# Performance work log

Hardware: AMD Instinct MI355X
Metric: run time of the kernel (lower is better)

## Reference

```python
import jax, jax.numpy as jnp
import numpy as np


def setup_inputs() -> dict:
    key = jax.random.key(0)
    ks = jax.random.split(key, 8)
    B, N, D, S = 4, 16384, 512, 512
    x = jax.random.normal(ks[0], (B, N, D), dtype=jnp.float32)
    jx = jnp.sort(jax.random.randint(ks[1], (N,), 0, S, dtype=jnp.int64))
    scale = 1.0 / np.sqrt(D)
    Wf = jax.random.normal(ks[2], (D, D), dtype=jnp.float32) * scale
    bf = jax.random.normal(ks[3], (D,), dtype=jnp.float32) * scale
    Wg = jax.random.normal(ks[4], (D, D), dtype=jnp.float32) * scale
    bg = jax.random.normal(ks[5], (D,), dtype=jnp.float32) * scale
    Wh = jax.random.normal(ks[6], (D, D), dtype=jnp.float32) * scale
    bh = jax.random.normal(ks[7], (D,), dtype=jnp.float32) * scale
    return {"x": x, "jx": jx, "num_segments": S, "Wf": Wf, "bf": bf,
            "Wg": Wg, "bg": bg, "Wh": Wh, "bh": bh}


def reference(x, jx, num_segments, Wf, bf, Wg, bg, Wh, bh):
    # x: [B, N, D]; jx: [N] segment ids; segments along axis 1.
    fx = jnp.einsum('bnd,ed->bne', x, Wf) + bf  # f(x)
    gx = jnp.einsum('bnd,ed->bne', x, Wg) + bg  # g(x)
    # move N to leading axis so jax.ops.segment_* apply: [N, B, D]
    gx_t = jnp.transpose(gx, (1, 0, 2))
    fx_t = jnp.transpose(fx, (1, 0, 2))
    # scatter_softmax over segments (numerically stable)
    m = jax.ops.segment_max(gx_t, jx, num_segments=num_segments)  # [S, B, D]
    e = jnp.exp(gx_t - m[jx])
    denom = jax.ops.segment_sum(e, jx, num_segments=num_segments)  # [S, B, D]
    w = e / denom[jx]  # [N, B, D]
    # weighted scatter-sum
    y_t = jax.ops.segment_sum(fx_t * w, jx, num_segments=num_segments)  # [S, B, D]
    y = jnp.transpose(y_t, (1, 0, 2))  # [B, S, D]
    hy = jnp.einsum('bsd,ed->bse', y, Wh) + bh
    # expand=True: gather back to per-element
    return hy[:, jx]  # [B, N, D]
```

## Files before the change

kernel.cpp:

```cpp
#include <hip/hip_runtime.h>
#include <stdint.h>

#define B_ 4
#define N_ 16384
#define D_ 512
#define S_ 512

typedef __attribute__((ext_vector_type(8))) short bf16x8;
typedef __attribute__((ext_vector_type(4))) float f32x4;

__device__ __forceinline__ float bf2f(unsigned short u) {
  union { unsigned int i; float f; } v; v.i = ((unsigned int)u) << 16; return v.f;
}
__device__ __forceinline__ unsigned short f2bf(float f) {
  unsigned int x = __float_as_uint(f);
  return (unsigned short)((x + 0x7FFFu + ((x >> 16) & 1u)) >> 16);
}
__device__ __forceinline__ float ldf(const void* p, long i, bool f32) {
  return f32 ? ((const float*)p)[i] : bf2f(((const unsigned short*)p)[i]);
}
__device__ __forceinline__ void gl_lds16(void* lds_base, const void* g) {
  __builtin_amdgcn_global_load_lds(
      (const __attribute__((address_space(1))) unsigned int*)g,
      (__attribute__((address_space(3))) unsigned int*)lds_base,
      16, 0, 0);
}

__device__ __forceinline__ bool jx_is_i64(const int* jx32) { return jx32[N_ - 1] == 0; }
__device__ __forceinline__ int seg_id(const int* jx32, int n, bool i64) {
  return i64 ? jx32[2 * n] : jx32[n];
}

__global__ void detect_f32(const unsigned short* __restrict__ x, int* __restrict__ flag) {
  __shared__ int cnt[256];
  int c = 0;
#pragma unroll
  for (int i = 0; i < 8; i++) {
    unsigned short w = x[threadIdx.x * 8 + i];
    int e = (w >> 7) & 0xFF;
    if (e == 0 || (e >= 100 && e <= 140)) c++;
  }
  cnt[threadIdx.x] = c;
  __syncthreads();
  for (int s = 128; s > 0; s >>= 1) {
    if ((int)threadIdx.x < s) cnt[threadIdx.x] += cnt[threadIdx.x + s];
    __syncthreads();
  }
  if (threadIdx.x == 0) *flag = (cnt[0] < (2048 * 9) / 10) ? 1 : 0;
}

__global__ void seg_bounds(const int* __restrict__ jx, int* __restrict__ st) {
  int s = blockIdx.x * blockDim.x + threadIdx.x;
  if (s > S_) return;
  bool i64 = jx_is_i64(jx);
  int lo = 0, hi = N_;
  while (lo < hi) {
    int mid = (lo + hi) >> 1;
    if (seg_id(jx, mid, i64) < s) lo = mid + 1; else hi = mid;
  }
  st[s] = lo;
}

__global__ void prep(const void* __restrict__ Wf, const void* __restrict__ bfv,
                     const void* __restrict__ Wg, const void* __restrict__ bgv,
                     const void* __restrict__ Wh, const void* __restrict__ bhv,
                     const int* __restrict__ flag,
                     unsigned short* __restrict__ Wfg, unsigned short* __restrict__ biasfg,
                     unsigned short* __restrict__ Whb, unsigned short* __restrict__ bhb) {
  const bool f32 = *flag != 0;
  int idx = blockIdx.x * 256 + threadIdx.x;
  if (idx < 524288) {
    int e = idx >> 9, d = idx & 511;
    float v = (e < 512) ? ldf(Wf, (long)e * 512 + d, f32)
                        : ldf(Wg, (long)(e - 512) * 512 + d, f32);
    Wfg[idx] = f2bf(v);
  } else if (idx < 786432) {
    Whb[idx - 524288] = f2bf(ldf(Wh, idx - 524288, f32));
  } else if (idx < 787456) {
    int j = idx - 786432;
    biasfg[j] = f2bf(j < 512 ? ldf(bfv, j, f32) : ldf(bgv, j - 512, f32));
  } else if (idx < 787968) {
    bhb[idx - 787456] = f2bf(ldf(bhv, idx - 787456, f32));
  }
}

__global__ __launch_bounds__(256)
void cvt_x(const void* __restrict__ x, const int* __restrict__ flag,
           unsigned short* __restrict__ xb) {
  const bool f32 = *flag != 0;
  const size_t i0 = ((size_t)blockIdx.x * 256 + threadIdx.x) * 8;
  bf16x8 v;
  if (f32) {
    const float4* p = (const float4*)((const float*)x + i0);
    float4 a = p[0], b = p[1];
    v[0]=f2bf(a.x); v[1]=f2bf(a.y); v[2]=f2bf(a.z); v[3]=f2bf(a.w);
    v[4]=f2bf(b.x); v[5]=f2bf(b.y); v[6]=f2bf(b.z); v[7]=f2bf(b.w);
  } else {
    v = *(const bf16x8*)((const unsigned short*)x + i0);
  }
  *(bf16x8*)(xb + i0) = v;
}

#define BK 32

__global__ __launch_bounds__(256, 2)
void gemm_bt(const unsigned short* __restrict__ A, const unsigned short* __restrict__ Bm,
             const unsigned short* __restrict__ bias,
             unsigned short* __restrict__ Cf, unsigned short* __restrict__ Cg,
             int E, int Kdim, int splitcol, int tilesM, int tilesN) {
  __shared__ __align__(16) unsigned short As[128 * BK];
  __shared__ __align__(16) unsigned short Bs[128 * BK];
  const int L = blockIdx.x;
  const int xcd = L & 7, local = L >> 3;
  const int rowsPerX = tilesM >> 3;
  const int tm = xcd * rowsPerX + local / tilesN;
  const int tn = local % tilesN;
  const int m0 = tm * 128, n0 = tn * 128;

  const int tid  = threadIdx.x;
  const int w    = tid >> 6;
  const int lane = tid & 63;
  const int wm   = w >> 1, wn = w & 1;
  const int l15  = lane & 15, l4 = lane >> 4;
  const int srow = lane >> 2;
  const int scol = (lane & 3) * 8;

  f32x4 acc[4][4];
#pragma unroll
  for (int i = 0; i < 4; i++)
#pragma unroll
    for (int j = 0; j < 4; j++) acc[i][j] = (f32x4){0.f, 0.f, 0.f, 0.f};

  for (int kt = 0; kt < Kdim; kt += BK) {
    __syncthreads();
#pragma unroll
    for (int r = 0; r < 2; r++) {
      const int rb = (r * 4 + w) * 16;
      gl_lds16(&As[rb * BK], A + (size_t)(m0 + rb + srow) * Kdim + kt + scol);
      gl_lds16(&Bs[rb * BK], Bm + (size_t)(n0 + rb + srow) * Kdim + kt + scol);
    }
    __syncthreads();

    bf16x8 a[4], b[4];
#pragma unroll
    for (int i = 0; i < 4; i++)
      a[i] = *(const bf16x8*)&As[(wm * 64 + i * 16 + l15) * BK + l4 * 8];
#pragma unroll
    for (int j = 0; j < 4; j++)
      b[j] = *(const bf16x8*)&Bs[(wn * 64 + j * 16 + l15) * BK + l4 * 8];
#pragma unroll
    for (int i = 0; i < 4; i++)
#pragma unroll
      for (int j = 0; j < 4; j++)
        acc[i][j] = __builtin_amdgcn_mfma_f32_16x16x32_bf16(a[i], b[j], acc[i][j], 0, 0, 0);
  }

#pragma unroll
  for (int j = 0; j < 4; j++) {
    const int col = n0 + wn * 64 + j * 16 + l15;
    const float bv = bf2f(bias[col]);
    unsigned short* base; int cc, stride;
    if (col < splitcol) { base = Cf; cc = col; stride = splitcol; }
    else { base = Cg; cc = col - splitcol; stride = E - splitcol; }
#pragma unroll
    for (int i = 0; i < 4; i++) {
      const int rowb = m0 + wm * 64 + i * 16 + l4 * 4;
#pragma unroll
      for (int r = 0; r < 4; r++)
        base[(size_t)(rowb + r) * stride + cc] = f2bf(acc[i][j][r] + bv);
    }
  }
}

__global__ __launch_bounds__(256)
void seg_softmax(const unsigned short* __restrict__ f, const unsigned short* __restrict__ g,
                 const int* __restrict__ segst, unsigned short* __restrict__ y) {
  const int s = blockIdx.x, b = blockIdx.y;
  const int st = segst[s], en = segst[s + 1];
  const int d0 = threadIdx.x * 2;
  float den0 = 0.f, den1 = 0.f, y0 = 0.f, y1 = 0.f;
  for (int n = st; n < en; n++) {
    const size_t off = (size_t)(b * N_ + n) * 512 + d0;
    const unsigned int fp = *(const unsigned int*)(f + off);
    const unsigned int gp = *(const unsigned int*)(g + off);
    const float f0 = bf2f((unsigned short)fp), f1 = bf2f((unsigned short)(fp >> 16));
    const float g0 = bf2f((unsigned short)gp), g1 = bf2f((unsigned short)(gp >> 16));
    const float e0 = __expf(g0), e1 = __expf(g1);
    den0 += e0; den1 += e1;
    y0 += f0 * e0; y1 += f1 * e1;
  }
  const float r0 = (en > st) ? y0 / den0 : 0.f;
  const float r1 = (en > st) ? y1 / den1 : 0.f;
  unsigned short* yr = y + (size_t)(b * S_ + s) * 512 + d0;
  yr[0] = f2bf(r0);
  yr[1] = f2bf(r1);
}

__global__ __launch_bounds__(256)
void gather_out(const unsigned short* __restrict__ hy, const int* __restrict__ jx,
                void* __restrict__ out, const int* __restrict__ flag) {
  const bool f32 = *flag != 0;
  const int gid  = blockIdx.x * 256 + threadIdx.x;
  const int wid  = gid >> 6;
  const int lane = gid & 63;
  const int b = wid >> 14;
  const int n = wid & (N_ - 1);
  const bool i64 = jx_is_i64(jx);
  const int s = seg_id(jx, n, i64);
  const bf16x8 v = *(const bf16x8*)(hy + (size_t)(b * S_ + s) * 512 + lane * 8);
  if (f32) {
    float* dst = (float*)out + (size_t)wid * 512 + lane * 8;
#pragma unroll
    for (int t = 0; t < 8; t++) dst[t] = bf2f((unsigned short)v[t]);
  } else {
    *(bf16x8*)((unsigned short*)out + (size_t)wid * 512 + lane * 8) = v;
  }
}

extern "C" void kernel_launch(void* const* d_in, const int* in_sizes, int n_in,
                              void* d_out, int out_size, void* d_ws, size_t ws_size,
                              hipStream_t stream) {
  const void* x  = d_in[0];
  const int* jx  = (const int*)d_in[1];
  const void* Wf = d_in[3];
  const void* bf = d_in[4];
  const void* Wg = d_in[5];
  const void* bg = d_in[6];
  const void* Wh = d_in[7];
  const void* bh = d_in[8];

  char* ws = (char*)d_ws;
  int* flag              = (int*)(ws + 0);
  int* segst             = (int*)(ws + 4096);
  unsigned short* biasfg = (unsigned short*)(ws + 8192);
  unsigned short* bhb    = (unsigned short*)(ws + 16384);
  unsigned short* Wfg    = (unsigned short*)(ws + 32768);
  unsigned short* Whb    = (unsigned short*)(ws + 1081344);
  unsigned short* y_ws   = (unsigned short*)(ws + 1605632);
  unsigned short* hy_ws  = (unsigned short*)(ws + 3702784);
  unsigned short* xb     = (unsigned short*)(ws + 8388608);
  unsigned short* fbuf   = (unsigned short*)d_out;
  unsigned short* gbuf   = (unsigned short*)d_out + (size_t)B_ * N_ * D_;

  detect_f32<<<1, 256, 0, stream>>>((const unsigned short*)x, flag);
  seg_bounds<<<3, 256, 0, stream>>>(jx, segst);
  prep<<<3078, 256, 0, stream>>>(Wf, bf, Wg, bg, Wh, bh, flag, Wfg, biasfg, Whb, bhb);
  cvt_x<<<16384, 256, 0, stream>>>(x, flag, xb);
  gemm_bt<<<4096, 256, 0, stream>>>(xb, Wfg, biasfg, fbuf, gbuf,
                                    1024, 512, 512, 512, 8);
  seg_softmax<<<dim3(S_, B_), 256, 0, stream>>>(fbuf, gbuf, segst, y_ws);
  gemm_bt<<<64, 256, 0, stream>>>(y_ws, Whb, bhb, hy_ws, hy_ws,
                                  512, 512, 512, 16, 4);
  gather_out<<<16384, 256, 0, stream>>>(hy_ws, jx, d_out, flag);
}
```

Before: 399.1 us.

## Fuse segment softmax-weighted reduction into f/g GEMM epilogue with atomics

Interleaves the Wf and Wg rows so each GEMM tile holds matching f and g columns. The epilogue computes exp(g)*f and exp(g), reduces them per segment inside the tile and atomically adds them into a float numerator/denominator buffer. A small kernel then divides to form y. The aim is to stop writing and re-reading the full bf16 f and g intermediates and to drop the separate softmax pass. Detection, segment-bound and prep launches are also merged into one kernel. In exchange it adds a memset, atomic contention and a per-block dtype classification, and it drops the max subtraction, which was already absent before.

Measured after the change: 428.9 us. 7.5% more time.

```diff
diff --git a/kernel.cpp b/kernel.cpp
--- a/kernel.cpp
+++ b/kernel.cpp
@@ -26,13 +26,7 @@
       16, 0, 0);
 }
 
-__device__ __forceinline__ bool jx_is_i64(const int* jx32) { return jx32[N_ - 1] == 0; }
-__device__ __forceinline__ int seg_id(const int* jx32, int n, bool i64) {
-  return i64 ? jx32[2 * n] : jx32[n];
-}
-
-__global__ void detect_f32(const unsigned short* __restrict__ x, int* __restrict__ flag) {
-  __shared__ int cnt[256];
+__device__ __forceinline__ bool classify_f32(const unsigned short* x, int* cnt) {
   int c = 0;
 #pragma unroll
   for (int i = 0; i < 8; i++) {
@@ -46,76 +40,78 @@
     if ((int)threadIdx.x < s) cnt[threadIdx.x] += cnt[threadIdx.x + s];
     __syncthreads();
   }
-  if (threadIdx.x == 0) *flag = (cnt[0] < (2048 * 9) / 10) ? 1 : 0;
-}
-
-__global__ void seg_bounds(const int* __restrict__ jx, int* __restrict__ st) {
-  int s = blockIdx.x * blockDim.x + threadIdx.x;
-  if (s > S_) return;
-  bool i64 = jx_is_i64(jx);
-  int lo = 0, hi = N_;
-  while (lo < hi) {
-    int mid = (lo + hi) >> 1;
-    if (seg_id(jx, mid, i64) < s) lo = mid + 1; else hi = mid;
-  }
-  st[s] = lo;
-}
-
-__global__ void prep(const void* __restrict__ Wf, const void* __restrict__ bfv,
-                     const void* __restrict__ Wg, const void* __restrict__ bgv,
-                     const void* __restrict__ Wh, const void* __restrict__ bhv,
-                     const int* __restrict__ flag,
-                     unsigned short* __restrict__ Wfg, unsigned short* __restrict__ biasfg,
-                     unsigned short* __restrict__ Whb, unsigned short* __restrict__ bhb) {
-  const bool f32 = *flag != 0;
-  int idx = blockIdx.x * 256 + threadIdx.x;
-  if (idx < 524288) {
-    int e = idx >> 9, d = idx & 511;
-    float v = (e < 512) ? ldf(Wf, (long)e * 512 + d, f32)
-                        : ldf(Wg, (long)(e - 512) * 512 + d, f32);
-    Wfg[idx] = f2bf(v);
-  } else if (idx < 786432) {
-    Whb[idx - 524288] = f2bf(ldf(Wh, idx - 524288, f32));
-  } else if (idx < 787456) {
-    int j = idx - 786432;
-    biasfg[j] = f2bf(j < 512 ? ldf(bfv, j, f32) : ldf(bgv, j - 512, f32));
-  } else if (idx < 787968) {
-    bhb[idx - 787456] = f2bf(ldf(bhv, idx - 787456, f32));
-  }
+  bool f32 = cnt[0] < 1843;
+  __syncthreads();
+  return f32;
+}
+
+__device__ __forceinline__ bool jx_is_i64(const int* jx32) { return jx32[N_ - 1] == 0; }
+__device__ __forceinline__ int seg_id(const int* jx32, int n, bool i64) {
+  return i64 ? jx32[2 * n] : jx32[n];
 }
 
 __global__ __launch_bounds__(256)
-void cvt_x(const void* __restrict__ x, const int* __restrict__ flag,
-           unsigned short* __restrict__ xb) {
-  const bool f32 = *flag != 0;
-  const size_t i0 = ((size_t)blockIdx.x * 256 + threadIdx.x) * 8;
-  bf16x8 v;
-  if (f32) {
-    const float4* p = (const float4*)((const float*)x + i0);
-    float4 a = p[0], b = p[1];
-    v[0]=f2bf(a.x); v[1]=f2bf(a.y); v[2]=f2bf(a.z); v[3]=f2bf(a.w);
-    v[4]=f2bf(b.x); v[5]=f2bf(b.y); v[6]=f2bf(b.z); v[7]=f2bf(b.w);
+void prep_all(const void* __restrict__ x, const int* __restrict__ jx,
+              const void* __restrict__ Wf, const void* __restrict__ bfv,
+              const void* __restrict__ Wg, const void* __restrict__ bgv,
+              const void* __restrict__ Wh, const void* __restrict__ bhv,
+              unsigned short* __restrict__ xb, unsigned short* __restrict__ Wfg,
+              unsigned short* __restrict__ biasfg, unsigned short* __restrict__ Whb,
+              unsigned short* __restrict__ bhb) {
+  const int blk = blockIdx.x, tid = threadIdx.x;
+  __shared__ int cnt[256];
+  const bool f32 = classify_f32((const unsigned short*)x, cnt);
+  if (blk < 16384) {
+    const size_t i0 = ((size_t)blk * 256 + tid) * 8;
+    bf16x8 v;
+    if (f32) {
+      const float4* p = (const float4*)((const float*)x + i0);
+      float4 a = p[0], b = p[1];
+      v[0]=f2bf(a.x); v[1]=f2bf(a.y); v[2]=f2bf(a.z); v[3]=f2bf(a.w);
+      v[4]=f2bf(b.x); v[5]=f2bf(b.y); v[6]=f2bf(b.z); v[7]=f2bf(b.w);
+    } else {
+      v = *(const bf16x8*)((const unsigned short*)x + i0);
+    }
+    *(bf16x8*)(xb + i0) = v;
   } else {
-    v = *(const bf16x8*)((const unsigned short*)x + i0);
-  }
-  *(bf16x8*)(xb + i0) = v;
+    int idx = (blk - 16384) * 256 + tid;
+    if (idx < 524288) {
+      int e = idx >> 9, dcol = idx & 511;
+      int drow = e >> 1;
+      float v = (e & 1) ? ldf(Wg, (long)drow * 512 + dcol, f32)
+                        : ldf(Wf, (long)drow * 512 + dcol, f32);
+      Wfg[idx] = f2bf(v);
+    } else if (idx < 786432) {
+      Whb[idx - 524288] = f2bf(ldf(Wh, idx - 524288, f32));
+    } else if (idx < 787456) {
+      int j = idx - 786432;
+      biasfg[j] = f2bf((j & 1) ? ldf(bgv, j >> 1, f32) : ldf(bfv, j >> 1, f32));
+    } else if (idx < 787968) {
+      bhb[idx - 787456] = f2bf(ldf(bhv, idx - 787456, f32));
+    }
+  }
 }
 
 #define BK 32
 
 __global__ __launch_bounds__(256, 2)
-void gemm_bt(const unsigned short* __restrict__ A, const unsigned short* __restrict__ Bm,
-             const unsigned short* __restrict__ bias,
-             unsigned short* __restrict__ Cf, unsigned short* __restrict__ Cg,
-             int E, int Kdim, int splitcol, int tilesM, int tilesN) {
-  __shared__ __align__(16) unsigned short As[128 * BK];
-  __shared__ __align__(16) unsigned short Bs[128 * BK];
+void gemm_fg_fused(const unsigned short* __restrict__ A,
+                   const unsigned short* __restrict__ Bm,
+                   const unsigned short* __restrict__ bias,
+                   const int* __restrict__ jx,
+                   float* __restrict__ nd) {
+  __shared__ __align__(16) char smem[16384];
+  unsigned short* As = (unsigned short*)smem;
+  unsigned short* Bs = (unsigned short*)(smem + 8192);
+  float2* red = (float2*)smem;
+
   const int L = blockIdx.x;
   const int xcd = L & 7, local = L >> 3;
-  const int rowsPerX = tilesM >> 3;
-  const int tm = xcd * rowsPerX + local / tilesN;
-  const int tn = local % tilesN;
+  const int tm = xcd * 64 + local / 8;
+  const int tn = local % 8;
   const int m0 = tm * 128, n0 = tn * 128;
+  const int b = m0 >> 14;
+  const int nbase = m0 & (N_ - 1);
 
   const int tid  = threadIdx.x;
   const int w    = tid >> 6;
@@ -131,6 +127,106 @@
 #pragma unroll
     for (int j = 0; j < 4; j++) acc[i][j] = (f32x4){0.f, 0.f, 0.f, 0.f};
 
+  for (int kt = 0; kt < 512; kt += BK) {
+    __syncthreads();
+#pragma unroll
+    for (int r = 0; r < 2; r++) {
+      const int rb = (r * 4 + w) * 16;
+      gl_lds16(&As[rb * BK], A + (size_t)(m0 + rb + srow) * 512 + kt + scol);
+      gl_lds16(&Bs[rb * BK], Bm + (size_t)(n0 + rb + srow) * 512 + kt + scol);
+    }
+    __syncthreads();
+
+    bf16x8 a[4], bb[4];
+#pragma unroll
+    for (int i = 0; i < 4; i++)
+      a[i] = *(const bf16x8*)&As[(wm * 64 + i * 16 + l15) * BK + l4 * 8];
+#pragma unroll
+    for (int j = 0; j < 4; j++)
+      bb[j] = *(const bf16x8*)&Bs[(wn * 64 + j * 16 + l15) * BK + l4 * 8];
+#pragma unroll
+    for (int i = 0; i < 4; i++)
+#pragma unroll
+      for (int j = 0; j < 4; j++)
+        acc[i][j] = __builtin_amdgcn_mfma_f32_16x16x32_bf16(a[i], bb[j], acc[i][j], 0, 0, 0);
+  }
+
+  const bool i64 = jx_is_i64(jx);
+  const bool evenlane = (l15 & 1) == 0;
+  const int slot_w = wn * 8 + (l15 >> 1);
+  for (int j = 0; j < 4; j++) {
+    __syncthreads();
+    const int col = n0 + wn * 64 + j * 16 + l15;
+    const float bv = bf2f(bias[col]);
+#pragma unroll
+    for (int i = 0; i < 4; i++) {
+#pragma unroll
+      for (int r = 0; r < 4; r++) {
+        const float val = acc[i][j][r] + bv;
+        const float partner = __shfl_xor(val, 1);
+        if (evenlane) {
+          const float e = __expf(partner);
+          const int row = wm * 64 + i * 16 + l4 * 4 + r;
+          red[row * 16 + slot_w] = make_float2(val * e, e);
+        }
+      }
+    }
+    __syncthreads();
+    if (tid < 128) {
+      const int slot = tid & 15, chunk = tid >> 4;
+      const int dg = (n0 >> 1) + (slot >> 3) * 32 + j * 8 + (slot & 7);
+      const int rbase = chunk * 16;
+      float nsum = 0.f, dsum = 0.f;
+      int cur = seg_id(jx, nbase + rbase, i64);
+      for (int k = 0; k < 16; k++) {
+        const int sg = seg_id(jx, nbase + rbase + k, i64);
+        const float2 v = red[(rbase + k) * 16 + slot];
+        if (sg != cur) {
+          float* t = nd + (((size_t)(b * S_ + cur)) * 512 + dg) * 2;
+          atomicAdd(t, nsum); atomicAdd(t + 1, dsum);
+          nsum = 0.f; dsum = 0.f; cur = sg;
+        }
+        nsum += v.x; dsum += v.y;
+      }
+      float* t = nd + (((size_t)(b * S_ + cur)) * 512 + dg) * 2;
+      atomicAdd(t, nsum); atomicAdd(t + 1, dsum);
+    }
+  }
+}
+
+__global__ __launch_bounds__(256)
+void y_div(const float* __restrict__ nd, unsigned short* __restrict__ y) {
+  const size_t i0 = ((size_t)blockIdx.x * 256 + threadIdx.x) * 2;
+  const float4 v = *(const float4*)(nd + i0 * 2);
+  unsigned int o = (unsigned int)f2bf(v.y > 0.f ? v.x / v.y : 0.f)
+                 | ((unsigned int)f2bf(v.w > 0.f ? v.z / v.w : 0.f) << 16);
+  *(unsigned int*)(y + i0) = o;
+}
+
+__global__ __launch_bounds__(256, 2)
+void gemm_bt(const unsigned short* __restrict__ A, const unsigned short* __restrict__ Bm,
+             const unsigned short* __restrict__ bias, unsigned short* __restrict__ C,
+             int E, int Kdim, int tilesM, int tilesN) {
+  __shared__ __align__(16) unsigned short As[128 * BK];
+  __shared__ __align__(16) unsigned short Bs[128 * BK];
+  const int L = blockIdx.x;
+  const int xcd = L & 7, local = L >> 3;
+  const int tm = xcd * (tilesM >> 3) + local / tilesN;
+  const int tn = local % tilesN;
+  const int m0 = tm * 128, n0 = tn * 128;
+  const int tid  = threadIdx.x;
+  const int w    = tid >> 6;
+  const int lane = tid & 63;
+  const int wm   = w >> 1, wn = w & 1;
+  const int l15  = lane & 15, l4 = lane >> 4;
+  const int srow = lane >> 2, scol = (lane & 3) * 8;
+
+  f32x4 acc[4][4];
+#pragma unroll
+  for (int i = 0; i < 4; i++)
+#pragma unroll
+    for (int j = 0; j < 4; j++) acc[i][j] = (f32x4){0.f, 0.f, 0.f, 0.f};
+
   for (int kt = 0; kt < Kdim; kt += BK) {
     __syncthreads();
 #pragma unroll
@@ -140,66 +236,38 @@
       gl_lds16(&Bs[rb * BK], Bm + (size_t)(n0 + rb + srow) * Kdim + kt + scol);
     }
     __syncthreads();
-
-    bf16x8 a[4], b[4];
+    bf16x8 a[4], bb[4];
 #pragma unroll
     for (int i = 0; i < 4; i++)
       a[i] = *(const bf16x8*)&As[(wm * 64 + i * 16 + l15) * BK + l4 * 8];
 #pragma unroll
     for (int j = 0; j < 4; j++)
-      b[j] = *(const bf16x8*)&Bs[(wn * 64 + j * 16 + l15) * BK + l4 * 8];
+      bb[j] = *(const bf16x8*)&Bs[(wn * 64 + j * 16 + l15) * BK + l4 * 8];
 #pragma unroll
     for (int i = 0; i < 4; i++)
 #pragma unroll
       for (int j = 0; j < 4; j++)
-        acc[i][j] = __builtin_amdgcn_mfma_f32_16x16x32_bf16(a[i], b[j], acc[i][j], 0, 0, 0);
-  }
-
+        acc[i][j] = __builtin_amdgcn_mfma_f32_16x16x32_bf16(a[i], bb[j], acc[i][j], 0, 0, 0);
+  }
 #pragma unroll
   for (int j = 0; j < 4; j++) {
     const int col = n0 + wn * 64 + j * 16 + l15;
     const float bv = bf2f(bias[col]);
-    unsigned short* base; int cc, stride;
-    if (col < splitcol) { base = Cf; cc = col; stride = splitcol; }
-    else { base = Cg; cc = col - splitcol; stride = E - splitcol; }
 #pragma unroll
     for (int i = 0; i < 4; i++) {
       const int rowb = m0 + wm * 64 + i * 16 + l4 * 4;
 #pragma unroll
       for (int r = 0; r < 4; r++)
-        base[(size_t)(rowb + r) * stride + cc] = f2bf(acc[i][j][r] + bv);
-    }
-  }
-}
-
-__global__ __launch_bounds__(256)
-void seg_softmax(const unsigned short* __restrict__ f, const unsigned short* __restrict__ g,
-                 const int* __restrict__ segst, unsigned short* __restrict__ y) {
-  const int s = blockIdx.x, b = blockIdx.y;
-  const int st = segst[s], en = segst[s + 1];
-  const int d0 = threadIdx.x * 2;
-  float den0 = 0.f, den1 = 0.f, y0 = 0.f, y1 = 0.f;
-  for (int n = st; n < en; n++) {
-    const size_t off = (size_t)(b * N_ + n) * 512 + d0;
-    const unsigned int fp = *(const unsigned int*)(f + off);
-    const unsigned int gp = *(const unsigned int*)(g + off);
-    const float f0 = bf2f((unsigned short)fp), f1 = bf2f((unsigned short)(fp >> 16));
-    const float g0 = bf2f((unsigned short)gp), g1 = bf2f((unsigned short)(gp >> 16));
-    const float e0 = __expf(g0), e1 = __expf(g1);
-    den0 += e0; den1 += e1;
-    y0 += f0 * e0; y1 += f1 * e1;
-  }
-  const float r0 = (en > st) ? y0 / den0 : 0.f;
-  const float r1 = (en > st) ? y1 / den1 : 0.f;
-  unsigned short* yr = y + (size_t)(b * S_ + s) * 512 + d0;
-  yr[0] = f2bf(r0);
-  yr[1] = f2bf(r1);
+        C[(size_t)(rowb + r) * E + col] = f2bf(acc[i][j][r] + bv);
+    }
+  }
 }
 
 __global__ __launch_bounds__(256)
 void gather_out(const unsigned short* __restrict__ hy, const int* __restrict__ jx,
-                void* __restrict__ out, const int* __restrict__ flag) {
-  const bool f32 = *flag != 0;
+                void* __restrict__ out, const void* __restrict__ x) {
+  __shared__ int cnt[256];
+  const bool f32 = classify_f32((const unsigned short*)x, cnt);
   const int gid  = blockIdx.x * 256 + threadIdx.x;
   const int wid  = gid >> 6;
   const int lane = gid & 63;
@@ -210,8 +278,13 @@
   const bf16x8 v = *(const bf16x8*)(hy + (size_t)(b * S_ + s) * 512 + lane * 8);
   if (f32) {
     float* dst = (float*)out + (size_t)wid * 512 + lane * 8;
-#pragma unroll
-    for (int t = 0; t < 8; t++) dst[t] = bf2f((unsigned short)v[t]);
+    float4 lo, hi;
+    lo.x=bf2f((unsigned short)v[0]); lo.y=bf2f((unsigned short)v[1]);
+    lo.z=bf2f((unsigned short)v[2]); lo.w=bf2f((unsigned short)v[3]);
+    hi.x=bf2f((unsigned short)v[4]); hi.y=bf2f((unsigned short)v[5]);
+    hi.z=bf2f((unsigned short)v[6]); hi.w=bf2f((unsigned short)v[7]);
+    *(float4*)dst = lo;
+    *(float4*)(dst + 4) = hi;
   } else {
     *(bf16x8*)((unsigned short*)out + (size_t)wid * 512 + lane * 8) = v;
   }
@@ -230,26 +303,20 @@
   const void* bh = d_in[8];
 
   char* ws = (char*)d_ws;
-  int* flag              = (int*)(ws + 0);
-  int* segst             = (int*)(ws + 4096);
   unsigned short* biasfg = (unsigned short*)(ws + 8192);
   unsigned short* bhb    = (unsigned short*)(ws + 16384);
   unsigned short* Wfg    = (unsigned short*)(ws + 32768);
   unsigned short* Whb    = (unsigned short*)(ws + 1081344);
   unsigned short* y_ws   = (unsigned short*)(ws + 1605632);
   unsigned short* hy_ws  = (unsigned short*)(ws + 3702784);
-  unsigned short* xb     = (unsigned short*)(ws + 8388608);
-  unsigned short* fbuf   = (unsigned short*)d_out;
-  unsigned short* gbuf   = (unsigned short*)d_out + (size_t)B_ * N_ * D_;
-
-  detect_f32<<<1, 256, 0, stream>>>((const unsigned short*)x, flag);
-  seg_bounds<<<3, 256, 0, stream>>>(jx, segst);
-  prep<<<3078, 256, 0, stream>>>(Wf, bf, Wg, bg, Wh, bh, flag, Wfg, biasfg, Whb, bhb);
-  cvt_x<<<16384, 256, 0, stream>>>(x, flag, xb);
-  gemm_bt<<<4096, 256, 0, stream>>>(xb, Wfg, biasfg, fbuf, gbuf,
-                                    1024, 512, 512, 512, 8);
-  seg_softmax<<<dim3(S_, B_), 256, 0, stream>>>(fbuf, gbuf, segst, y_ws);
-  gemm_bt<<<64, 256, 0, stream>>>(y_ws, Whb, bhb, hy_ws, hy_ws,
-                                  512, 512, 512, 16, 4);
-  gather_out<<<16384, 256, 0, stream>>>(hy_ws, jx, d_out, flag);
-}
+  float*          nd     = (float*)(ws + 8388608);
+  unsigned short* xb     = (unsigned short*)d_out;
+
+  hipMemsetAsync(nd, 0, (size_t)B_ * S_ * D_ * 2 * sizeof(float), stream);
+  prep_all<<<19462, 256, 0, stream>>>(x, jx, Wf, bf, Wg, bg, Wh, bh,
+                                      xb, Wfg, biasfg, Whb, bhb);
+  gemm_fg_fused<<<4096, 256, 0, stream>>>(xb, Wfg, biasfg, jx, nd);
+  y_div<<<2048, 256, 0, stream>>>(nd, y_ws);
+  gemm_bt<<<64, 256, 0, stream>>>(y_ws, Whb, bhb, hy_ws, 512, 512, 16, 4);
+  gather_out<<<16384, 256, 0, stream>>>(hy_ws, jx, d_out, x);
+}
```
